# Kernel tuning notes

Measured on AMD Instinct MI355X. Metric: run time of the kernel, lower is better.

## Reference

```python
import jax, jax.numpy as jnp
import numpy as np

N = 100000
E = 1600000
D_IN = 64
D_HID = 64
D_OUT = 64
R = 8
BN_EPS = 1e-5


def setup_inputs() -> dict:
    key = jax.random.key(0)
    ks = jax.random.split(key, 12)
    x = jax.random.normal(ks[0], (N, D_IN), dtype=jnp.float32)
    edge_index = jax.random.randint(ks[1], (2, E), 0, N, dtype=jnp.int64)
    edge_type = jax.random.randint(ks[2], (E,), 0, R, dtype=jnp.int64)
    s1 = 1.0 / np.sqrt(D_IN)
    s2 = 1.0 / np.sqrt(D_HID)
    w1 = jax.random.uniform(ks[3], (R, D_IN, D_HID), jnp.float32, -s1, s1)
    root1 = jax.random.uniform(ks[4], (D_IN, D_HID), jnp.float32, -s1, s1)
    b1 = jnp.zeros((D_HID,), jnp.float32)
    gamma1 = jnp.ones((D_HID,), jnp.float32)
    beta1 = jnp.zeros((D_HID,), jnp.float32)
    w2 = jax.random.uniform(ks[5], (R, D_HID, D_OUT), jnp.float32, -s2, s2)
    root2 = jax.random.uniform(ks[6], (D_HID, D_OUT), jnp.float32, -s2, s2)
    b2 = jnp.zeros((D_OUT,), jnp.float32)
    return {"x": x, "edge_index": edge_index, "edge_type": edge_type,
            "w1": w1, "root1": root1, "b1": b1, "gamma1": gamma1, "beta1": beta1,
            "w2": w2, "root2": root2, "b2": b2}


def rgcn_conv(x, edge_index, edge_type, W, root, bias):
    # PyG RGCNConv with aggr='mean': per relation r, mean of neighbor features
    # over incoming edges of type r, transformed by W[r]; plus root transform + bias.
    # Aggregate-then-transform (legal since transform is linear): one fused
    # segment_sum keyed by (dst, relation), then a grouped GEMM via einsum.
    n, d = x.shape
    src, dst = edge_index[0], edge_index[1]
    seg = dst * R + edge_type                     # [E] combined segment id
    msg = x[src]                                  # [E, d] gather
    agg = jax.ops.segment_sum(msg, seg, num_segments=n * R).reshape(n, R, d)
    cnt = jax.ops.segment_sum(jnp.ones((src.shape[0],), x.dtype), seg,
                              num_segments=n * R).reshape(n, R, 1)
    mean = agg / jnp.maximum(cnt, 1.0)            # [n, R, d]
    return jnp.einsum('nrd,rdo->no', mean, W) + x @ root + bias


def batch_norm(h, gamma, beta):
    mu = h.mean(axis=0)
    var = h.var(axis=0)
    return gamma * (h - mu) * jax.lax.rsqrt(var + BN_EPS) + beta


def reference(x, edge_index, edge_type, w1, root1, b1, gamma1, beta1, w2, root2, b2):
    h = rgcn_conv(x, edge_index, edge_type, w1, root1, b1)
    h = jax.nn.relu(batch_norm(h, gamma1, beta1))
    # dropout: identity (eval mode)
    out = rgcn_conv(h, edge_index, edge_type, w2, root2, b2)
    return out
```

## Files before the change

### kernel.cpp

```cpp
#include <hip/hip_runtime.h>
#include <hip/hip_bf16.h>

#define NN 100000
#define EE 1600000
#define RR 8
#define DD 64
#define MM (NN * RR)
#define BN_EPS 1e-5f
#define KTOT 576
#define BSTRIDE 584

#define NB 391
#define EPB 8192
#define NBIN ((EE + EPB - 1) / EPB)

typedef __bf16 bf16x8 __attribute__((ext_vector_type(8)));
typedef float  f32x4  __attribute__((ext_vector_type(4)));

static __device__ __forceinline__ unsigned short f32_to_bf16(float f) {
    unsigned int u = __float_as_uint(f);
    unsigned int r = u + 0x7FFFu + ((u >> 16) & 1u);
    return (unsigned short)(r >> 16);
}
static __device__ __forceinline__ float bflo(unsigned int u) {
    return __uint_as_float(u << 16);
}
static __device__ __forceinline__ float bfhi(unsigned int u) {
    return __uint_as_float(u & 0xFFFF0000u);
}


__global__ void k_bcount(const int* __restrict__ dst, int* __restrict__ btot) {
    __shared__ int cnt[NB];
    int t = threadIdx.x;
    for (int i = t; i < NB; i += 256) cnt[i] = 0;
    __syncthreads();
    int base = blockIdx.x * EPB;
#pragma unroll
    for (int i = 0; i < EPB / 256; ++i) {
        int e = base + i * 256 + t;
        if (e < EE) atomicAdd(&cnt[dst[e] >> 8], 1);
    }
    __syncthreads();
    for (int i = t; i < NB; i += 256)
        if (cnt[i]) atomicAdd(&btot[i], cnt[i]);
}

__global__ void k_bscan(const int* __restrict__ btot, int* __restrict__ bbase,
                        int* __restrict__ gcur, int* __restrict__ rowptr) {
    __shared__ int sd[512];
    int t = threadIdx.x;
    int v = (t < NB) ? btot[t] : 0;
    sd[t] = v;
    __syncthreads();
    for (int off = 1; off < 512; off <<= 1) {
        int x = (t >= off) ? sd[t - off] : 0;
        __syncthreads();
        sd[t] += x;
        __syncthreads();
    }
    if (t < NB) { bbase[t] = sd[t] - v; gcur[t] = sd[t] - v; }
    if (t == NB - 1) { bbase[NB] = sd[t]; rowptr[MM] = sd[t]; }
}

__global__ void k_bin(const int* __restrict__ src, const int* __restrict__ dst,
                      const int* __restrict__ et, int* __restrict__ gcur,
                      unsigned int* __restrict__ ebuf) {
    __shared__ int cnt[NB];
    __shared__ int bas[NB];
    __shared__ int off[NB];
    int t = threadIdx.x;
    for (int i = t; i < NB; i += 256) { cnt[i] = 0; off[i] = 0; }
    __syncthreads();
    int base = blockIdx.x * EPB;
#pragma unroll
    for (int i = 0; i < EPB / 256; ++i) {
        int e = base + i * 256 + t;
        if (e < EE) atomicAdd(&cnt[dst[e] >> 8], 1);
    }
    __syncthreads();
    for (int i = t; i < NB; i += 256) {
        int c = cnt[i];
        bas[i] = c ? atomicAdd(&gcur[i], c) : 0;
    }
    __syncthreads();
#pragma unroll
    for (int i = 0; i < EPB / 256; ++i) {
        int e = base + i * 256 + t;
        if (e < EE) {
            int d = dst[e];
            int b = d >> 8;
            int lk = ((d & 255) << 3) | et[e];
            unsigned int rec0 = (unsigned int)src[e] | ((unsigned int)lk << 17);
            int p = bas[b] + atomicAdd(&off[b], 1);
            ebuf[p] = rec0;
        }
    }
}

__global__ __launch_bounds__(256) void k_bcsr(const int* __restrict__ bbase,
                                              const unsigned int* __restrict__ ebuf,
                                              int* __restrict__ rowptr,
                                              int* __restrict__ rec) {
    __shared__ int deg[2048];
    __shared__ int part[256];
    int b = blockIdx.x, t = threadIdx.x;
    int e0 = bbase[b], e1 = bbase[b + 1];
    for (int i = t; i < 2048; i += 256) deg[i] = 0;
    __syncthreads();
    for (int e = e0 + t; e < e1; e += 256) atomicAdd(&deg[ebuf[e] >> 17], 1);
    __syncthreads();
    int loc[8];
    int s = 0;
#pragma unroll
    for (int j = 0; j < 8; ++j) { loc[j] = deg[t * 8 + j]; s += loc[j]; }
    part[t] = s;
    __syncthreads();
    for (int off = 1; off < 256; off <<= 1) {
        int x = (t >= off) ? part[t - off] : 0;
        __syncthreads();
        part[t] += x;
        __syncthreads();
    }
    int run = part[t] - s;
    int keyBase = b * 2048;
#pragma unroll
    for (int j = 0; j < 8; ++j) {
        int g = keyBase + t * 8 + j;
        if (g < MM) rowptr[g] = e0 + run;
        deg[t * 8 + j] = run;
        run += loc[j];
    }
    __syncthreads();
    for (int e = e0 + t; e < e1; e += 256) {
        unsigned int v = ebuf[e];
        int lk = v >> 17;
        int pos = e0 + atomicAdd(&deg[lk], 1);
        rec[pos] = (int)(v & 0x1FFFFu);
    }
}


__global__ void k_tobf16(const float* __restrict__ X, unsigned short* __restrict__ Xb) {
    int i = blockIdx.x * 256 + threadIdx.x;
    if (i >= NN * DD / 4) return;
    float4 v = ((const float4*)X)[i];
    ushort4 o;
    o.x = f32_to_bf16(v.x); o.y = f32_to_bf16(v.y);
    o.z = f32_to_bf16(v.z); o.w = f32_to_bf16(v.w);
    ((ushort4*)Xb)[i] = o;
}


__global__ void k_prepw(const float* __restrict__ W, const float* __restrict__ Root,
                        unsigned short* __restrict__ WcT) {
    int i = blockIdx.x * 256 + threadIdx.x;
    if (i >= 64 * KTOT) return;
    int o = i / KTOT;
    int k = i - o * KTOT;
    float v;
    if (k < 512) v = W[(size_t)(k >> 6) * 4096 + (k & 63) * 64 + o];
    else         v = Root[(k - 512) * 64 + o];
    WcT[(size_t)o * KTOT + k] = f32_to_bf16(v);
}


__global__ __launch_bounds__(256, 4) void k_fused(const unsigned short* __restrict__ Xb,
                                                  const int* __restrict__ rowptr,
                                                  const int* __restrict__ rec,
                                                  const unsigned short* __restrict__ WcT,
                                                  const float* __restrict__ bias,
                                                  float* __restrict__ Out,
                                                  float* __restrict__ stats,
                                                  int dostats) {
    __shared__ unsigned short Atile[32 * BSTRIDE];
    __shared__ float ssum[4][32];
    __shared__ float ssq[4][32];
    int t = threadIdx.x;
    int wv = t >> 6, lane = t & 63;
    int r = lane >> 3;
    int q = lane & 7;
    int nodeBase = blockIdx.x * 32 + wv * 8;
    int base8 = nodeBase * RR;
    int v0 = rowptr[base8 + lane];
    int v1 = rowptr[base8 + lane + 1];

    {
        int i = lane >> 3, c = lane & 7;
        uint4 xv = *(const uint4*)(Xb + (size_t)(nodeBase + i) * DD + c * 8);
        *(uint4*)(Atile + (size_t)(wv * 8 + i) * BSTRIDE + 512 + c * 8) = xv;
    }

#pragma unroll 1
    for (int i = 0; i < 8; ++i) {
        int e0 = __shfl(v0, i * 8 + r);
        int e1 = __shfl(v1, i * 8 + r);
        float a0[8] = {0,0,0,0,0,0,0,0};
        float a1[8] = {0,0,0,0,0,0,0,0};
        float a2[8] = {0,0,0,0,0,0,0,0};
        float a3[8] = {0,0,0,0,0,0,0,0};
        int e = e0;
        for (; e + 3 < e1; e += 4) {
            int s0 = rec[e], s1 = rec[e + 1], s2 = rec[e + 2], s3 = rec[e + 3];
            uint4 u0 = *(const uint4*)(Xb + (size_t)s0 * DD + q * 8);
            uint4 u1 = *(const uint4*)(Xb + (size_t)s1 * DD + q * 8);
            uint4 u2 = *(const uint4*)(Xb + (size_t)s2 * DD + q * 8);
            uint4 u3 = *(const uint4*)(Xb + (size_t)s3 * DD + q * 8);
            a0[0] += bflo(u0.x); a0[1] += bfhi(u0.x); a0[2] += bflo(u0.y); a0[3] += bfhi(u0.y);
            a0[4] += bflo(u0.z); a0[5] += bfhi(u0.z); a0[6] += bflo(u0.w); a0[7] += bfhi(u0.w);
            a1[0] += bflo(u1.x); a1[1] += bfhi(u1.x); a1[2] += bflo(u1.y); a1[3] += bfhi(u1.y);
            a1[4] += bflo(u1.z); a1[5] += bfhi(u1.z); a1[6] += bflo(u1.w); a1[7] += bfhi(u1.w);
            a2[0] += bflo(u2.x); a2[1] += bfhi(u2.x); a2[2] += bflo(u2.y); a2[3] += bfhi(u2.y);
            a2[4] += bflo(u2.z); a2[5] += bfhi(u2.z); a2[6] += bflo(u2.w); a2[7] += bfhi(u2.w);
            a3[0] += bflo(u3.x); a3[1] += bfhi(u3.x); a3[2] += bflo(u3.y); a3[3] += bfhi(u3.y);
            a3[4] += bflo(u3.z); a3[5] += bfhi(u3.z); a3[6] += bflo(u3.w); a3[7] += bfhi(u3.w);
        }
        if (e + 1 < e1) {
            int s0 = rec[e], s1 = rec[e + 1];
            uint4 u0 = *(const uint4*)(Xb + (size_t)s0 * DD + q * 8);
            uint4 u1 = *(const uint4*)(Xb + (size_t)s1 * DD + q * 8);
            a0[0] += bflo(u0.x); a0[1] += bfhi(u0.x); a0[2] += bflo(u0.y); a0[3] += bfhi(u0.y);
            a0[4] += bflo(u0.z); a0[5] += bfhi(u0.z); a0[6] += bflo(u0.w); a0[7] += bfhi(u0.w);
            a1[0] += bflo(u1.x); a1[1] += bfhi(u1.x); a1[2] += bflo(u1.y); a1[3] += bfhi(u1.y);
            a1[4] += bflo(u1.z); a1[5] += bfhi(u1.z); a1[6] += bflo(u1.w); a1[7] += bfhi(u1.w);
            e += 2;
        }
        if (e < e1) {
            int s0 = rec[e];
            uint4 u0 = *(const uint4*)(Xb + (size_t)s0 * DD + q * 8);
            a0[0] += bflo(u0.x); a0[1] += bfhi(u0.x); a0[2] += bflo(u0.y); a0[3] += bfhi(u0.y);
            a0[4] += bflo(u0.z); a0[5] += bfhi(u0.z); a0[6] += bflo(u0.w); a0[7] += bfhi(u0.w);
        }
        int cnt = e1 - e0;
        float inv = 1.0f / (float)(cnt > 1 ? cnt : 1);
        uint4 o;
        o.x = (unsigned)f32_to_bf16((a0[0]+a1[0]+a2[0]+a3[0]) * inv) | ((unsigned)f32_to_bf16((a0[1]+a1[1]+a2[1]+a3[1]) * inv) << 16);
        o.y = (unsigned)f32_to_bf16((a0[2]+a1[2]+a2[2]+a3[2]) * inv) | ((unsigned)f32_to_bf16((a0[3]+a1[3]+a2[3]+a3[3]) * inv) << 16);
        o.z = (unsigned)f32_to_bf16((a0[4]+a1[4]+a2[4]+a3[4]) * inv) | ((unsigned)f32_to_bf16((a0[5]+a1[5]+a2[5]+a3[5]) * inv) << 16);
        o.w = (unsigned)f32_to_bf16((a0[6]+a1[6]+a2[6]+a3[6]) * inv) | ((unsigned)f32_to_bf16((a0[7]+a1[7]+a2[7]+a3[7]) * inv) << 16);
        *(uint4*)(Atile + (size_t)(wv * 8 + i) * BSTRIDE + lane * 8) = o;
    }
    __syncthreads();

    int m16 = lane & 15, quad = lane >> 4;
    int rt = wv >> 1, ch = wv & 1;
    const unsigned short* as = Atile + (rt * 16 + m16) * BSTRIDE + quad * 8;
    const unsigned short* bg = WcT + (size_t)(ch * 32 + m16) * KTOT + quad * 8;
    union AU { uint4 u; bf16x8 f; };
    f32x4 acc[2];
    acc[0] = (f32x4){0.f, 0.f, 0.f, 0.f};
    acc[1] = (f32x4){0.f, 0.f, 0.f, 0.f};
#pragma unroll
    for (int kb = 0; kb < 18; ++kb) {
        AU av, b0, b1;
        av.u = *(const uint4*)(as + kb * 32);
        b0.u = *(const uint4*)(bg + kb * 32);
        b1.u = *(const uint4*)(bg + 16 * KTOT + kb * 32);
        acc[0] = __builtin_amdgcn_mfma_f32_16x16x32_bf16(av.f, b0.f, acc[0], 0, 0, 0);
        acc[1] = __builtin_amdgcn_mfma_f32_16x16x32_bf16(av.f, b1.f, acc[1], 0, 0, 0);
    }

    int row0 = blockIdx.x * 32 + rt * 16 + quad * 4;
#pragma unroll
    for (int nt = 0; nt < 2; ++nt) {
        int col = ch * 32 + nt * 16 + m16;
        float bb = bias[col];
        float s = 0.f, sq = 0.f;
#pragma unroll
        for (int i2 = 0; i2 < 4; ++i2) {
            float v = acc[nt][i2] + bb;
            Out[(size_t)(row0 + i2) * 64 + col] = v;
            s += v; sq += v * v;
        }
        if (dostats) {
            s += __shfl_xor(s, 16); s += __shfl_xor(s, 32);
            sq += __shfl_xor(sq, 16); sq += __shfl_xor(sq, 32);
            if (quad == 0) { ssum[wv][nt * 16 + m16] = s; ssq[wv][nt * 16 + m16] = sq; }
        }
    }
    if (dostats) {
        __syncthreads();
        if (t < 64) {
            int half = t >> 5, cl = t & 31;
            atomicAdd(&stats[t], ssum[half][cl] + ssum[half + 2][cl]);
        } else if (t < 128) {
            int c2 = t - 64;
            int half = c2 >> 5, cl = c2 & 31;
            atomicAdd(&stats[64 + c2], ssq[half][cl] + ssq[half + 2][cl]);
        }
    }
}


__global__ void k_bnrelu(const float* __restrict__ H, unsigned short* __restrict__ Hb,
                         const float* __restrict__ stats,
                         const float* __restrict__ gamma, const float* __restrict__ beta) {
    int idx = blockIdx.x * 256 + threadIdx.x;
    const int total = NN * DD / 4;
    if (idx >= total) return;
    int c0 = (idx & 15) * 4;
    float4 v = ((const float4*)H)[idx];
    float inv = 1.0f / (float)NN;
    float4 o;
    {
        float mu = stats[c0 + 0] * inv;
        float var = stats[64 + c0 + 0] * inv - mu * mu;
        float sc = gamma[c0 + 0] * rsqrtf(var + BN_EPS);
        float r = sc * (v.x - mu) + beta[c0 + 0];
        o.x = r > 0.f ? r : 0.f;
    }
    {
        float mu = stats[c0 + 1] * inv;
        float var = stats[64 + c0 + 1] * inv - mu * mu;
        float sc = gamma[c0 + 1] * rsqrtf(var + BN_EPS);
        float r = sc * (v.y - mu) + beta[c0 + 1];
        o.y = r > 0.f ? r : 0.f;
    }
    {
        float mu = stats[c0 + 2] * inv;
        float var = stats[64 + c0 + 2] * inv - mu * mu;
        float sc = gamma[c0 + 2] * rsqrtf(var + BN_EPS);
        float r = sc * (v.z - mu) + beta[c0 + 2];
        o.z = r > 0.f ? r : 0.f;
    }
    {
        float mu = stats[c0 + 3] * inv;
        float var = stats[64 + c0 + 3] * inv - mu * mu;
        float sc = gamma[c0 + 3] * rsqrtf(var + BN_EPS);
        float r = sc * (v.w - mu) + beta[c0 + 3];
        o.w = r > 0.f ? r : 0.f;
    }
    ushort4 ob;
    ob.x = f32_to_bf16(o.x); ob.y = f32_to_bf16(o.y);
    ob.z = f32_to_bf16(o.z); ob.w = f32_to_bf16(o.w);
    ((ushort4*)Hb)[idx] = ob;
}


static inline size_t alignup(size_t x) { return (x + 255) & ~(size_t)255; }

extern "C" void kernel_launch(void* const* d_in, const int* in_sizes, int n_in,
                              void* d_out, int out_size, void* d_ws, size_t ws_size,
                              hipStream_t stream) {
    const float* x      = (const float*)d_in[0];
    const int*   eidx   = (const int*)d_in[1];
    const int*   etype  = (const int*)d_in[2];
    const float* w1     = (const float*)d_in[3];
    const float* root1  = (const float*)d_in[4];
    const float* b1     = (const float*)d_in[5];
    const float* gamma1 = (const float*)d_in[6];
    const float* beta1  = (const float*)d_in[7];
    const float* w2     = (const float*)d_in[8];
    const float* root2  = (const float*)d_in[9];
    const float* b2     = (const float*)d_in[10];
    float* out = (float*)d_out;

    const int* src = eidx;
    const int* dst = eidx + EE;

    char* w = (char*)d_ws;
    int* rowptr = (int*)w;            w += alignup((size_t)(MM + 1) * 4);
    int* btot   = (int*)w;            w += alignup(512 * 4);
    int* bbase  = (int*)w;            w += alignup(512 * 4);
    int* gcur   = (int*)w;            w += alignup(512 * 4);
    int* rec    = (int*)w;            w += alignup((size_t)EE * 4);
    float* h    = (float*)w;          w += alignup((size_t)NN * DD * 4);
    unsigned short* xhb = (unsigned short*)w; w += alignup((size_t)NN * DD * 2);
    unsigned short* wct1 = (unsigned short*)w; w += alignup((size_t)64 * KTOT * 2);
    unsigned short* wct2 = (unsigned short*)w; w += alignup((size_t)64 * KTOT * 2);
    float* stats = (float*)w;         w += alignup(128 * 4);
    unsigned int* ebuf = (unsigned int*)h;

    hipMemsetAsync(btot, 0, 512 * 4, stream);
    hipMemsetAsync(stats, 0, 128 * 4, stream);

    k_prepw<<<dim3(144), dim3(256), 0, stream>>>(w1, root1, wct1);
    k_prepw<<<dim3(144), dim3(256), 0, stream>>>(w2, root2, wct2);
    k_tobf16<<<dim3(NN * DD / 4 / 256 + 1), dim3(256), 0, stream>>>(x, xhb);

    k_bcount<<<dim3(NBIN), dim3(256), 0, stream>>>(dst, btot);
    k_bscan<<<dim3(1), dim3(512), 0, stream>>>(btot, bbase, gcur, rowptr);
    k_bin<<<dim3(NBIN), dim3(256), 0, stream>>>(src, dst, etype, gcur, ebuf);
    k_bcsr<<<dim3(NB), dim3(256), 0, stream>>>(bbase, ebuf, rowptr, rec);

    k_fused<<<dim3(NN / 32), dim3(256), 0, stream>>>(xhb, rowptr, rec, wct1, b1, h, stats, 1);
    k_bnrelu<<<dim3(NN * DD / 4 / 256), dim3(256), 0, stream>>>(h, xhb, stats, gamma1, beta1);

    k_fused<<<dim3(NN / 32), dim3(256), 0, stream>>>(xhb, rowptr, rec, wct2, b2, out, stats, 0);
}
```

Measured before the change: 451.6 us.

## Halve fused block tile to 16 nodes and raise occupancy target

Each block of the fused gather+GEMM kernel now handles 16 nodes instead of 32. Each wave gathers 4 nodes and computes one 16-column MFMA slice, and twice as many blocks are launched. The launch-bounds occupancy hint rises to 8 and LDS per block halves, so more waves per CU can hide the latency of the irregular gathers. The trade-off is twice as many BN-stat atomics, now issued per wave directly without a shared-memory reduction, more register pressure, and weight tiles re-read by more blocks.

```diff
diff --git a/kernel.cpp b/kernel.cpp
--- a/kernel.cpp
+++ b/kernel.cpp
@@ -165,7 +165,7 @@
 }
 
 
-__global__ __launch_bounds__(256, 4) void k_fused(const unsigned short* __restrict__ Xb,
+__global__ __launch_bounds__(256, 8) void k_fused(const unsigned short* __restrict__ Xb,
                                                   const int* __restrict__ rowptr,
                                                   const int* __restrict__ rec,
                                                   const unsigned short* __restrict__ WcT,
@@ -173,28 +173,25 @@
                                                   float* __restrict__ Out,
                                                   float* __restrict__ stats,
                                                   int dostats) {
-    __shared__ unsigned short Atile[32 * BSTRIDE];
-    __shared__ float ssum[4][32];
-    __shared__ float ssq[4][32];
+    __shared__ unsigned short Atile[16 * BSTRIDE];
     int t = threadIdx.x;
     int wv = t >> 6, lane = t & 63;
     int r = lane >> 3;
     int q = lane & 7;
-    int nodeBase = blockIdx.x * 32 + wv * 8;
-    int base8 = nodeBase * RR;
-    int v0 = rowptr[base8 + lane];
-    int v1 = rowptr[base8 + lane + 1];
-
-    {
+    int nodeBase = blockIdx.x * 16;
+    int wnode = nodeBase + wv * 4;
+    int v0 = rowptr[wnode * RR + (lane < 33 ? lane : 32)];
+
+    if (lane < 32) {
         int i = lane >> 3, c = lane & 7;
-        uint4 xv = *(const uint4*)(Xb + (size_t)(nodeBase + i) * DD + c * 8);
-        *(uint4*)(Atile + (size_t)(wv * 8 + i) * BSTRIDE + 512 + c * 8) = xv;
+        uint4 xv = *(const uint4*)(Xb + (size_t)(wnode + i) * DD + c * 8);
+        *(uint4*)(Atile + (size_t)(wv * 4 + i) * BSTRIDE + 512 + c * 8) = xv;
     }
 
 #pragma unroll 1
-    for (int i = 0; i < 8; ++i) {
+    for (int i = 0; i < 4; ++i) {
         int e0 = __shfl(v0, i * 8 + r);
-        int e1 = __shfl(v1, i * 8 + r);
+        int e1 = __shfl(v0, i * 8 + r + 1);
         float a0[8] = {0,0,0,0,0,0,0,0};
         float a1[8] = {0,0,0,0,0,0,0,0};
         float a2[8] = {0,0,0,0,0,0,0,0};
@@ -238,55 +235,39 @@
         o.y = (unsigned)f32_to_bf16((a0[2]+a1[2]+a2[2]+a3[2]) * inv) | ((unsigned)f32_to_bf16((a0[3]+a1[3]+a2[3]+a3[3]) * inv) << 16);
         o.z = (unsigned)f32_to_bf16((a0[4]+a1[4]+a2[4]+a3[4]) * inv) | ((unsigned)f32_to_bf16((a0[5]+a1[5]+a2[5]+a3[5]) * inv) << 16);
         o.w = (unsigned)f32_to_bf16((a0[6]+a1[6]+a2[6]+a3[6]) * inv) | ((unsigned)f32_to_bf16((a0[7]+a1[7]+a2[7]+a3[7]) * inv) << 16);
-        *(uint4*)(Atile + (size_t)(wv * 8 + i) * BSTRIDE + lane * 8) = o;
+        *(uint4*)(Atile + (size_t)(wv * 4 + i) * BSTRIDE + lane * 8) = o;
     }
     __syncthreads();
 
     int m16 = lane & 15, quad = lane >> 4;
-    int rt = wv >> 1, ch = wv & 1;
-    const unsigned short* as = Atile + (rt * 16 + m16) * BSTRIDE + quad * 8;
-    const unsigned short* bg = WcT + (size_t)(ch * 32 + m16) * KTOT + quad * 8;
+    const unsigned short* as = Atile + m16 * BSTRIDE + quad * 8;
+    const unsigned short* bg = WcT + (size_t)(wv * 16 + m16) * KTOT + quad * 8;
     union AU { uint4 u; bf16x8 f; };
-    f32x4 acc[2];
-    acc[0] = (f32x4){0.f, 0.f, 0.f, 0.f};
-    acc[1] = (f32x4){0.f, 0.f, 0.f, 0.f};
+    f32x4 acc = (f32x4){0.f, 0.f, 0.f, 0.f};
 #pragma unroll
     for (int kb = 0; kb < 18; ++kb) {
-        AU av, b0, b1;
+        AU av, bv;
         av.u = *(const uint4*)(as + kb * 32);
-        b0.u = *(const uint4*)(bg + kb * 32);
-        b1.u = *(const uint4*)(bg + 16 * KTOT + kb * 32);
-        acc[0] = __builtin_amdgcn_mfma_f32_16x16x32_bf16(av.f, b0.f, acc[0], 0, 0, 0);
-        acc[1] = __builtin_amdgcn_mfma_f32_16x16x32_bf16(av.f, b1.f, acc[1], 0, 0, 0);
-    }
-
-    int row0 = blockIdx.x * 32 + rt * 16 + quad * 4;
-#pragma unroll
-    for (int nt = 0; nt < 2; ++nt) {
-        int col = ch * 32 + nt * 16 + m16;
-        float bb = bias[col];
-        float s = 0.f, sq = 0.f;
-#pragma unroll
-        for (int i2 = 0; i2 < 4; ++i2) {
-            float v = acc[nt][i2] + bb;
-            Out[(size_t)(row0 + i2) * 64 + col] = v;
-            s += v; sq += v * v;
-        }
-        if (dostats) {
-            s += __shfl_xor(s, 16); s += __shfl_xor(s, 32);
-            sq += __shfl_xor(sq, 16); sq += __shfl_xor(sq, 32);
-            if (quad == 0) { ssum[wv][nt * 16 + m16] = s; ssq[wv][nt * 16 + m16] = sq; }
-        }
+        bv.u = *(const uint4*)(bg + kb * 32);
+        acc = __builtin_amdgcn_mfma_f32_16x16x32_bf16(av.f, bv.f, acc, 0, 0, 0);
+    }
+
+    int row0 = nodeBase + quad * 4;
+    int col = wv * 16 + m16;
+    float bb = bias[col];
+    float s = 0.f, sq = 0.f;
+#pragma unroll
+    for (int i2 = 0; i2 < 4; ++i2) {
+        float v = acc[i2] + bb;
+        Out[(size_t)(row0 + i2) * 64 + col] = v;
+        s += v; sq += v * v;
     }
     if (dostats) {
-        __syncthreads();
-        if (t < 64) {
-            int half = t >> 5, cl = t & 31;
-            atomicAdd(&stats[t], ssum[half][cl] + ssum[half + 2][cl]);
-        } else if (t < 128) {
-            int c2 = t - 64;
-            int half = c2 >> 5, cl = c2 & 31;
-            atomicAdd(&stats[64 + c2], ssq[half][cl] + ssq[half + 2][cl]);
+        s += __shfl_xor(s, 16); s += __shfl_xor(s, 32);
+        sq += __shfl_xor(sq, 16); sq += __shfl_xor(sq, 32);
+        if (quad == 0) {
+            atomicAdd(&stats[col], s);
+            atomicAdd(&stats[64 + col], sq);
         }
     }
 }
@@ -383,8 +364,8 @@
     k_bin<<<dim3(NBIN), dim3(256), 0, stream>>>(src, dst, etype, gcur, ebuf);
     k_bcsr<<<dim3(NB), dim3(256), 0, stream>>>(bbase, ebuf, rowptr, rec);
 
-    k_fused<<<dim3(NN / 32), dim3(256), 0, stream>>>(xhb, rowptr, rec, wct1, b1, h, stats, 1);
+    k_fused<<<dim3(NN / 16), dim3(256), 0, stream>>>(xhb, rowptr, rec, wct1, b1, h, stats, 1);
     k_bnrelu<<<dim3(NN * DD / 4 / 256), dim3(256), 0, stream>>>(h, xhb, stats, gamma1, beta1);
 
-    k_fused<<<dim3(NN / 32), dim3(256), 0, stream>>>(xhb, rowptr, rec, wct2, b2, out, stats, 0);
-}
+    k_fused<<<dim3(NN / 16), dim3(256), 0, stream>>>(xhb, rowptr, rec, wct2, b2, out, stats, 0);
+}
```

Result: no change. 452.6 us (+0.2%).
